# Kernel tuning notes

Hardware: AMD Instinct MI355X
Metric: run time of the kernel (lower is better)

## Reference

```python
import jax, jax.numpy as jnp
import numpy as np

B, D, H, K = 32768, 256, 8192, 32  # tokens, d_in, hidden latents, topk
EPS = float(np.finfo(np.float32).eps)


def setup_inputs() -> dict:
    key = jax.random.key(0)
    k0, k1, k2 = jax.random.split(key, 3)
    x = jax.random.normal(k0, (B, D), jnp.float32)
    W_enc = jax.random.normal(k1, (H, D), jnp.float32) * 0.02
    b_enc = jnp.zeros((H,), jnp.float32)
    # decoder initialized as encoder clone with unit-norm rows (set_decoder_norm_to_unit_norm)
    W_dec0 = jax.random.normal(k2, (H, D), jnp.float32) * 0.02
    W_dec = W_dec0 / (jnp.linalg.norm(W_dec0, axis=1, keepdims=True) + EPS)
    b_dec = jnp.zeros((D,), jnp.float32)
    return {"x": x, "W_enc": W_enc, "b_enc": b_enc, "W_dec": W_dec, "b_dec": b_dec}


def reference(x, W_enc, b_enc, W_dec, b_dec):
    # sae_in = x - b_dec; pre_acts = relu(encoder(sae_in))
    sae_in = x - b_dec
    pre_acts = jax.nn.relu(sae_in @ W_enc.T + b_enc)  # [B, H]
    # topk_activation: keep top-K values per row, zeros elsewhere; then z @ W_dec.
    # Equivalent (same math, no dense scatter): gather the K active decoder rows
    # and take the weighted sum.
    vals, idx = jax.lax.top_k(pre_acts, K)              # [B, K]
    x_reconstructed = jnp.einsum('bk,bkd->bd', vals, W_dec[idx]) + b_dec  # [B, D]
    return x_reconstructed
```

## Files before the change

### kernel.cpp

```cpp
#include <hip/hip_runtime.h>

#define B_TOK 32768
#define D_IN  256
#define H_LAT 8192
#define TOPK  32
#define MT    64
#define NT    128
#define NCH   (H_LAT / NT)
#define CAP   144
#define DELTA 0.016f

typedef __attribute__((ext_vector_type(4))) float f32x4;
typedef __attribute__((ext_vector_type(8))) short bf16x8;

__device__ __forceinline__ unsigned short f2bf(float f) {
    unsigned u = __float_as_uint(f);
    return (unsigned short)((u + 0x7fffu + ((u >> 16) & 1u)) >> 16);
}
__device__ __forceinline__ float bf2f(unsigned short u) {
    return __uint_as_float((unsigned)u << 16);
}

__global__ __launch_bounds__(256)
void conv_kernel(const float* __restrict__ W, unsigned short* __restrict__ Wbf,
                 float* __restrict__ s2w, const float* __restrict__ Wd,
                 unsigned short* __restrict__ Wdbf) {
    const int tid  = threadIdx.x;
    const int wave = tid >> 6, lane = tid & 63;
    const int l15 = lane & 15, quad = lane >> 4;
    const int ct16 = blockIdx.x * 4 + wave;

    float acc = 0.0f;
    {
        const float* src = W + (size_t)(ct16 * 16 + l15) * D_IN + quad * 8;
        unsigned short* dst = Wbf + ((size_t)ct16 * 8) * 512 + lane * 8;
#pragma unroll
        for (int c8 = 0; c8 < 8; ++c8) {
            const float4 v0 = *(const float4*)(src + c8 * 32);
            const float4 v1 = *(const float4*)(src + c8 * 32 + 4);
            acc += v0.x * v0.x + v0.y * v0.y + v0.z * v0.z + v0.w * v0.w +
                   v1.x * v1.x + v1.y * v1.y + v1.z * v1.z + v1.w * v1.w;
            ushort4 p0, p1;
            p0.x = f2bf(v0.x); p0.y = f2bf(v0.y); p0.z = f2bf(v0.z); p0.w = f2bf(v0.w);
            p1.x = f2bf(v1.x); p1.y = f2bf(v1.y); p1.z = f2bf(v1.z); p1.w = f2bf(v1.w);
            *(ushort4*)(dst + c8 * 512)     = p0;
            *(ushort4*)(dst + c8 * 512 + 4) = p1;
        }
    }
    {
        const int total4 = (H_LAT * D_IN) / 4;
        for (int i = blockIdx.x * blockDim.x + tid; i < total4; i += 128 * 256) {
            const float4 d = ((const float4*)Wd)[i];
            ushort4 od;
            od.x = f2bf(d.x); od.y = f2bf(d.y); od.z = f2bf(d.z); od.w = f2bf(d.w);
            ((ushort4*)Wdbf)[i] = od;
        }
    }
#pragma unroll
    for (int off = 32; off > 0; off >>= 1) acc += __shfl_down(acc, off, 64);
    if (lane == 0) atomicAdd(s2w, acc);
}

__global__ __launch_bounds__(512, 4)
void sae_main(const float* __restrict__ x, const float* __restrict__ W_enc,
              const float* __restrict__ b_enc, const float* __restrict__ b_dec,
              float* __restrict__ out,
              const unsigned short* __restrict__ Wbf, const float* __restrict__ s2w,
              const unsigned short* __restrict__ Wdbf) {
    __shared__ __align__(16) char smem[32768 + MT * CAP * 4];
    __shared__ int   cnt[MT];
    __shared__ float thr[MT];

    unsigned short* A = (unsigned short*)smem;
    auto pool = reinterpret_cast<unsigned (*)[CAP]>(smem + 32768);
    unsigned short* ext_i = (unsigned short*)smem;
    float*          ext_v = (float*)(smem + 1024);

    const int tid  = threadIdx.x;
    const int row0 = blockIdx.x * MT;
    const int wave = tid >> 6, lane = tid & 63;
    const int l15 = lane & 15, quad = lane >> 4;

    if (tid < MT) { cnt[tid] = 0; thr[tid] = 0.0f; }
    __syncthreads();

    {
        const int r = tid >> 3, q = tid & 7;
        const float* xr = x + (size_t)(row0 + r) * D_IN + q * 32;
        const float* bd = b_dec + q * 32;
        unsigned short* dst = A + ((r >> 4) * 8 + q) * 512 + (r & 15) * 8;
        float s2 = 0.0f;
#pragma unroll
        for (int j = 0; j < 4; ++j) {
            const float4 a = ((const float4*)xr)[2 * j];
            const float4 b = ((const float4*)xr)[2 * j + 1];
            const float4 da = ((const float4*)bd)[2 * j];
            const float4 db = ((const float4*)bd)[2 * j + 1];
            float v[8] = {a.x - da.x, a.y - da.y, a.z - da.z, a.w - da.w,
                          b.x - db.x, b.y - db.y, b.z - db.z, b.w - db.w};
            ushort4 p0, p1;
            p0.x = f2bf(v[0]); p0.y = f2bf(v[1]); p0.z = f2bf(v[2]); p0.w = f2bf(v[3]);
            p1.x = f2bf(v[4]); p1.y = f2bf(v[5]); p1.z = f2bf(v[6]); p1.w = f2bf(v[7]);
#pragma unroll
            for (int e = 0; e < 8; ++e) s2 += v[e] * v[e];
            *(ushort4*)(dst + j * 128)     = p0;
            *(ushort4*)(dst + j * 128 + 4) = p1;
        }
        atomicAdd(&thr[r], s2);
    }
    __syncthreads();
    if (tid < MT) {
        const float s2wm = s2w[0] * (1.0f / ((float)H_LAT * (float)D_IN));
        thr[tid] = 2.3f * sqrtf(s2wm * thr[tid]);
    }
    __syncthreads();

    float thrv[4][4];
#pragma unroll
    for (int mt = 0; mt < 4; ++mt)
#pragma unroll
        for (int qi = 0; qi < 4; ++qi) thrv[mt][qi] = thr[mt * 16 + quad * 4 + qi];

    const unsigned short* bp = Wbf + (size_t)(wave * 8) * 512 + lane * 8;
    const unsigned short* ap = A + lane * 8;
    const float* bep = b_enc + wave * 16 + l15;
    int col0 = wave * 16 + l15;

    int pos[4][4];
    auto collect = [&](const f32x4 (&ac)[4], int cbase) {
        const unsigned colk = (unsigned)(8191 - cbase);
#pragma unroll
        for (int mt = 0; mt < 4; ++mt)
#pragma unroll
            for (int qi = 0; qi < 4; ++qi) {
                pos[mt][qi] = -1;
                if (ac[mt][qi] > thrv[mt][qi])
                    pos[mt][qi] = atomicAdd(&cnt[mt * 16 + quad * 4 + qi], 1);
            }
#pragma unroll
        for (int mt = 0; mt < 4; ++mt)
#pragma unroll
            for (int qi = 0; qi < 4; ++qi) {
                if ((unsigned)pos[mt][qi] < CAP)
                    pool[mt * 16 + quad * 4 + qi][pos[mt][qi]] =
                        ((unsigned)f2bf(ac[mt][qi]) << 13) | colk;
            }
    };

    for (int g = 0; g < NCH; g += 4) {
        const float bv0 = bep[0],      bv1 = bep[NT];
        const float bv2 = bep[2 * NT], bv3 = bep[3 * NT];

        f32x4 acc0[4], acc1[4], acc2[4], acc3[4];
#pragma unroll
        for (int mt = 0; mt < 4; ++mt) {
            acc0[mt] = {bv0, bv0, bv0, bv0};
            acc1[mt] = {bv1, bv1, bv1, bv1};
            acc2[mt] = {bv2, bv2, bv2, bv2};
            acc3[mt] = {bv3, bv3, bv3, bv3};
        }

#pragma unroll
        for (int c8 = 0; c8 < 8; ++c8) {
            const bf16x8 a0 = *(const bf16x8*)(ap + (0 * 8 + c8) * 512);
            const bf16x8 a1 = *(const bf16x8*)(ap + (1 * 8 + c8) * 512);
            const bf16x8 a2 = *(const bf16x8*)(ap + (2 * 8 + c8) * 512);
            const bf16x8 a3 = *(const bf16x8*)(ap + (3 * 8 + c8) * 512);
            const bf16x8 w0 = *(const bf16x8*)(bp + c8 * 512);
            const bf16x8 w1 = *(const bf16x8*)(bp + 32768 + c8 * 512);
            const bf16x8 w2 = *(const bf16x8*)(bp + 65536 + c8 * 512);
            const bf16x8 w3 = *(const bf16x8*)(bp + 98304 + c8 * 512);
            acc0[0] = __builtin_amdgcn_mfma_f32_16x16x32_bf16(a0, w0, acc0[0], 0, 0, 0);
            acc0[1] = __builtin_amdgcn_mfma_f32_16x16x32_bf16(a1, w0, acc0[1], 0, 0, 0);
            acc0[2] = __builtin_amdgcn_mfma_f32_16x16x32_bf16(a2, w0, acc0[2], 0, 0, 0);
            acc0[3] = __builtin_amdgcn_mfma_f32_16x16x32_bf16(a3, w0, acc0[3], 0, 0, 0);
            acc1[0] = __builtin_amdgcn_mfma_f32_16x16x32_bf16(a0, w1, acc1[0], 0, 0, 0);
            acc1[1] = __builtin_amdgcn_mfma_f32_16x16x32_bf16(a1, w1, acc1[1], 0, 0, 0);
            acc1[2] = __builtin_amdgcn_mfma_f32_16x16x32_bf16(a2, w1, acc1[2], 0, 0, 0);
            acc1[3] = __builtin_amdgcn_mfma_f32_16x16x32_bf16(a3, w1, acc1[3], 0, 0, 0);
            acc2[0] = __builtin_amdgcn_mfma_f32_16x16x32_bf16(a0, w2, acc2[0], 0, 0, 0);
            acc2[1] = __builtin_amdgcn_mfma_f32_16x16x32_bf16(a1, w2, acc2[1], 0, 0, 0);
            acc2[2] = __builtin_amdgcn_mfma_f32_16x16x32_bf16(a2, w2, acc2[2], 0, 0, 0);
            acc2[3] = __builtin_amdgcn_mfma_f32_16x16x32_bf16(a3, w2, acc2[3], 0, 0, 0);
            acc3[0] = __builtin_amdgcn_mfma_f32_16x16x32_bf16(a0, w3, acc3[0], 0, 0, 0);
            acc3[1] = __builtin_amdgcn_mfma_f32_16x16x32_bf16(a1, w3, acc3[1], 0, 0, 0);
            acc3[2] = __builtin_amdgcn_mfma_f32_16x16x32_bf16(a2, w3, acc3[2], 0, 0, 0);
            acc3[3] = __builtin_amdgcn_mfma_f32_16x16x32_bf16(a3, w3, acc3[3], 0, 0, 0);
        }

        collect(acc0, col0);
        collect(acc1, col0 + NT);
        collect(acc2, col0 + 2 * NT);
        collect(acc3, col0 + 3 * NT);

        bp  += 4 * 32768;
        bep += 4 * NT;
        col0 += 4 * NT;
    }
    __syncthreads();

    unsigned short* ei = ext_i + wave * 64;
    float*          ev = ext_v + wave * 64;

    for (int rr = 0; rr < 8; ++rr) {
        const int r = wave * 8 + rr;
        const int n = min(cnt[r], CAP);

        unsigned p[3]; int rk[3];
        const int S = (n <= 128) ? 2 : 3;
#pragma unroll
        for (int e = 0; e < 3; ++e) {
            const int c = e * 64 + lane;
            p[e] = (c < n) ? pool[r][c] : (unsigned)(c + 1);
            rk[e] = 0;
        }
        if (S == 2) {
            for (int s = 0; s < 64; ++s) {
                const int src = (lane + s) & 63;
                const unsigned q0 = (unsigned)__shfl((int)p[0], src, 64);
                const unsigned q1 = (unsigned)__shfl((int)p[1], src, 64);
                rk[0] += (q0 > p[0]) + (q1 > p[0]);
                rk[1] += (q0 > p[1]) + (q1 > p[1]);
            }
        } else {
            for (int s = 0; s < 64; ++s) {
                const int src = (lane + s) & 63;
#pragma unroll
                for (int e = 0; e < 3; ++e) {
                    const unsigned q = (unsigned)__shfl((int)p[e], src, 64);
#pragma unroll
                    for (int a = 0; a < 3; ++a) rk[a] += (q > p[a]);
                }
            }
        }
#pragma unroll
        for (int e = 0; e < 3; ++e) {
            if (e < S && rk[e] < 64) {
                if (p[e] >= 8192u) {
                    ei[rk[e]] = (unsigned short)(8191 - (p[e] & 0x1fffu));
                    ev[rk[e]] = __uint_as_float((p[e] >> 13) << 16);
                } else {
                    ei[rk[e]] = (unsigned short)(0x2000 + rk[e]);
                    ev[rk[e]] = 0.0f;
                }
            }
        }

        const float v32 = ev[TOPK - 1];
        const float va  = ev[lane];
        const int   h   = ei[lane];
        float v = va;
        if (h < H_LAT && fabsf(va - v32) <= DELTA) {
            const float* xr  = x + (size_t)(row0 + r) * D_IN;
            const float* wr_ = W_enc + (size_t)h * D_IN;
            float s = 0.0f;
            for (int kk = 0; kk < D_IN / 4; ++kk) {
                const float4 xv = ((const float4*)xr)[kk];
                const float4 dv = ((const float4*)b_dec)[kk];
                const float4 wv = ((const float4*)wr_)[kk];
                s = fmaf(xv.x - dv.x, wv.x, s);
                s = fmaf(xv.y - dv.y, wv.y, s);
                s = fmaf(xv.z - dv.z, wv.z, s);
                s = fmaf(xv.w - dv.w, wv.w, s);
            }
            v = fmaxf(s + b_enc[h], 0.0f);
        }

        int rank = 0;
        for (int s = 0; s < 64; ++s) {
            const int src = (lane + s) & 63;
            const float wv = __shfl(v, src, 64);
            const int   wh = __shfl(h, src, 64);
            rank += (wv > v) || (wv == v && wh < h);
        }
        if (rank < TOPK) { ev[rank] = v; ei[rank] = (unsigned short)h; }

        const float4 bd4 = *(const float4*)&b_dec[lane * 4];
        float4 o = bd4;
#pragma unroll 8
        for (int k = 0; k < TOPK; ++k) {
            const float vv = ev[k];
            const int   hh = ei[k];
            if (hh < H_LAT) {
                const ushort4 w = *(const ushort4*)&Wdbf[(size_t)hh * D_IN + lane * 4];
                o.x = fmaf(vv, bf2f(w.x), o.x); o.y = fmaf(vv, bf2f(w.y), o.y);
                o.z = fmaf(vv, bf2f(w.z), o.z); o.w = fmaf(vv, bf2f(w.w), o.w);
            }
        }
        *(float4*)&out[(size_t)(row0 + r) * D_IN + lane * 4] = o;
    }
}

extern "C" void kernel_launch(void* const* d_in, const int* in_sizes, int n_in,
                              void* d_out, int out_size, void* d_ws, size_t ws_size,
                              hipStream_t stream) {
    const float* x     = (const float*)d_in[0];
    const float* W_enc = (const float*)d_in[1];
    const float* b_enc = (const float*)d_in[2];
    const float* W_dec = (const float*)d_in[3];
    const float* b_dec = (const float*)d_in[4];
    float* out = (float*)d_out;

    const size_t wel = (size_t)H_LAT * D_IN;
    float* s2w = (float*)d_ws;
    unsigned short* Wbf  = (unsigned short*)((char*)d_ws + 256);
    unsigned short* Wdbf = Wbf + wel;

    hipMemsetAsync(d_ws, 0, 256, stream);
    conv_kernel<<<dim3(128), dim3(256), 0, stream>>>(W_enc, Wbf, s2w, W_dec, Wdbf);
    sae_main<<<dim3(B_TOK / MT), dim3(512), 0, stream>>>(x, W_enc, b_enc, b_dec,
                                                         out, Wbf, s2w, Wdbf);
}
```

Baseline: 546.9 us.

## Software-pipeline encoder weight loads and widen conversion kernel grid

The main loop now handles two 128-column chunks per iteration instead of four. The weight fragments for the next k-step are prefetched into double-buffered registers while the current MFMAs run, which hides global load latency and lowers accumulator register pressure. The conversion kernel is relaunched with 512 blocks, each block splitting one 16-row tile across its waves, so the weight casts have more parallelism. The exact-refinement dot product loop is also unrolled. The risks are a different register allocation and more collect calls per chunk of work.

```diff
diff --git a/kernel.cpp b/kernel.cpp
--- a/kernel.cpp
+++ b/kernel.cpp
@@ -28,14 +28,15 @@
     const int tid  = threadIdx.x;
     const int wave = tid >> 6, lane = tid & 63;
     const int l15 = lane & 15, quad = lane >> 4;
-    const int ct16 = blockIdx.x * 4 + wave;
+    const int ct16 = blockIdx.x;
 
     float acc = 0.0f;
     {
         const float* src = W + (size_t)(ct16 * 16 + l15) * D_IN + quad * 8;
-        unsigned short* dst = Wbf + ((size_t)ct16 * 8) * 512 + lane * 8;
-#pragma unroll
-        for (int c8 = 0; c8 < 8; ++c8) {
+        unsigned short* dst = Wbf + (size_t)ct16 * 4096 + lane * 8;
+#pragma unroll
+        for (int cc = 0; cc < 2; ++cc) {
+            const int c8 = wave * 2 + cc;
             const float4 v0 = *(const float4*)(src + c8 * 32);
             const float4 v1 = *(const float4*)(src + c8 * 32 + 4);
             acc += v0.x * v0.x + v0.y * v0.y + v0.z * v0.z + v0.w * v0.w +
@@ -49,7 +50,7 @@
     }
     {
         const int total4 = (H_LAT * D_IN) / 4;
-        for (int i = blockIdx.x * blockDim.x + tid; i < total4; i += 128 * 256) {
+        for (int i = blockIdx.x * 256 + tid; i < total4; i += 512 * 256) {
             const float4 d = ((const float4*)Wd)[i];
             ushort4 od;
             od.x = f2bf(d.x); od.y = f2bf(d.y); od.z = f2bf(d.z); od.w = f2bf(d.w);
@@ -60,6 +61,24 @@
     for (int off = 32; off > 0; off >>= 1) acc += __shfl_down(acc, off, 64);
     if (lane == 0) atomicAdd(s2w, acc);
 }
+
+#define GSTEP(CW0, CW1, NW0, NW1, C8, NBASE, NC8)                              \
+    {                                                                          \
+        NW0 = *(const bf16x8*)((NBASE) + (NC8) * 512);                         \
+        NW1 = *(const bf16x8*)((NBASE) + 32768 + (NC8) * 512);                 \
+        const bf16x8 a0 = *(const bf16x8*)(ap + (0 * 8 + (C8)) * 512);         \
+        const bf16x8 a1 = *(const bf16x8*)(ap + (1 * 8 + (C8)) * 512);         \
+        const bf16x8 a2 = *(const bf16x8*)(ap + (2 * 8 + (C8)) * 512);         \
+        const bf16x8 a3 = *(const bf16x8*)(ap + (3 * 8 + (C8)) * 512);         \
+        acc0[0] = __builtin_amdgcn_mfma_f32_16x16x32_bf16(a0, CW0, acc0[0], 0, 0, 0); \
+        acc0[1] = __builtin_amdgcn_mfma_f32_16x16x32_bf16(a1, CW0, acc0[1], 0, 0, 0); \
+        acc0[2] = __builtin_amdgcn_mfma_f32_16x16x32_bf16(a2, CW0, acc0[2], 0, 0, 0); \
+        acc0[3] = __builtin_amdgcn_mfma_f32_16x16x32_bf16(a3, CW0, acc0[3], 0, 0, 0); \
+        acc1[0] = __builtin_amdgcn_mfma_f32_16x16x32_bf16(a0, CW1, acc1[0], 0, 0, 0); \
+        acc1[1] = __builtin_amdgcn_mfma_f32_16x16x32_bf16(a1, CW1, acc1[1], 0, 0, 0); \
+        acc1[2] = __builtin_amdgcn_mfma_f32_16x16x32_bf16(a2, CW1, acc1[2], 0, 0, 0); \
+        acc1[3] = __builtin_amdgcn_mfma_f32_16x16x32_bf16(a3, CW1, acc1[3], 0, 0, 0); \
+    }
 
 __global__ __launch_bounds__(512, 4)
 void sae_main(const float* __restrict__ x, const float* __restrict__ W_enc,
@@ -147,55 +166,35 @@
             }
     };
 
-    for (int g = 0; g < NCH; g += 4) {
-        const float bv0 = bep[0],      bv1 = bep[NT];
-        const float bv2 = bep[2 * NT], bv3 = bep[3 * NT];
-
-        f32x4 acc0[4], acc1[4], acc2[4], acc3[4];
+    bf16x8 wa0, wa1, wb0, wb1;
+    wa0 = *(const bf16x8*)(bp);
+    wa1 = *(const bf16x8*)(bp + 32768);
+
+    for (int g = 0; g < NCH; g += 2) {
+        const float bv0 = bep[0], bv1 = bep[NT];
+
+        f32x4 acc0[4], acc1[4];
 #pragma unroll
         for (int mt = 0; mt < 4; ++mt) {
             acc0[mt] = {bv0, bv0, bv0, bv0};
             acc1[mt] = {bv1, bv1, bv1, bv1};
-            acc2[mt] = {bv2, bv2, bv2, bv2};
-            acc3[mt] = {bv3, bv3, bv3, bv3};
-        }
-
-#pragma unroll
-        for (int c8 = 0; c8 < 8; ++c8) {
-            const bf16x8 a0 = *(const bf16x8*)(ap + (0 * 8 + c8) * 512);
-            const bf16x8 a1 = *(const bf16x8*)(ap + (1 * 8 + c8) * 512);
-            const bf16x8 a2 = *(const bf16x8*)(ap + (2 * 8 + c8) * 512);
-            const bf16x8 a3 = *(const bf16x8*)(ap + (3 * 8 + c8) * 512);
-            const bf16x8 w0 = *(const bf16x8*)(bp + c8 * 512);
-            const bf16x8 w1 = *(const bf16x8*)(bp + 32768 + c8 * 512);
-            const bf16x8 w2 = *(const bf16x8*)(bp + 65536 + c8 * 512);
-            const bf16x8 w3 = *(const bf16x8*)(bp + 98304 + c8 * 512);
-            acc0[0] = __builtin_amdgcn_mfma_f32_16x16x32_bf16(a0, w0, acc0[0], 0, 0, 0);
-            acc0[1] = __builtin_amdgcn_mfma_f32_16x16x32_bf16(a1, w0, acc0[1], 0, 0, 0);
-            acc0[2] = __builtin_amdgcn_mfma_f32_16x16x32_bf16(a2, w0, acc0[2], 0, 0, 0);
-            acc0[3] = __builtin_amdgcn_mfma_f32_16x16x32_bf16(a3, w0, acc0[3], 0, 0, 0);
-            acc1[0] = __builtin_amdgcn_mfma_f32_16x16x32_bf16(a0, w1, acc1[0], 0, 0, 0);
-            acc1[1] = __builtin_amdgcn_mfma_f32_16x16x32_bf16(a1, w1, acc1[1], 0, 0, 0);
-            acc1[2] = __builtin_amdgcn_mfma_f32_16x16x32_bf16(a2, w1, acc1[2], 0, 0, 0);
-            acc1[3] = __builtin_amdgcn_mfma_f32_16x16x32_bf16(a3, w1, acc1[3], 0, 0, 0);
-            acc2[0] = __builtin_amdgcn_mfma_f32_16x16x32_bf16(a0, w2, acc2[0], 0, 0, 0);
-            acc2[1] = __builtin_amdgcn_mfma_f32_16x16x32_bf16(a1, w2, acc2[1], 0, 0, 0);
-            acc2[2] = __builtin_amdgcn_mfma_f32_16x16x32_bf16(a2, w2, acc2[2], 0, 0, 0);
-            acc2[3] = __builtin_amdgcn_mfma_f32_16x16x32_bf16(a3, w2, acc2[3], 0, 0, 0);
-            acc3[0] = __builtin_amdgcn_mfma_f32_16x16x32_bf16(a0, w3, acc3[0], 0, 0, 0);
-            acc3[1] = __builtin_amdgcn_mfma_f32_16x16x32_bf16(a1, w3, acc3[1], 0, 0, 0);
-            acc3[2] = __builtin_amdgcn_mfma_f32_16x16x32_bf16(a2, w3, acc3[2], 0, 0, 0);
-            acc3[3] = __builtin_amdgcn_mfma_f32_16x16x32_bf16(a3, w3, acc3[3], 0, 0, 0);
-        }
+        }
+
+        GSTEP(wa0, wa1, wb0, wb1, 0, bp, 1);
+        GSTEP(wb0, wb1, wa0, wa1, 1, bp, 2);
+        GSTEP(wa0, wa1, wb0, wb1, 2, bp, 3);
+        GSTEP(wb0, wb1, wa0, wa1, 3, bp, 4);
+        GSTEP(wa0, wa1, wb0, wb1, 4, bp, 5);
+        GSTEP(wb0, wb1, wa0, wa1, 5, bp, 6);
+        GSTEP(wa0, wa1, wb0, wb1, 6, bp, 7);
+        GSTEP(wb0, wb1, wa0, wa1, 7, bp + 65536, 0);
 
         collect(acc0, col0);
         collect(acc1, col0 + NT);
-        collect(acc2, col0 + 2 * NT);
-        collect(acc3, col0 + 3 * NT);
-
-        bp  += 4 * 32768;
-        bep += 4 * NT;
-        col0 += 4 * NT;
+
+        bp  += 65536;
+        bep += 2 * NT;
+        col0 += 2 * NT;
     }
     __syncthreads();
 
@@ -254,6 +253,7 @@
             const float* xr  = x + (size_t)(row0 + r) * D_IN;
             const float* wr_ = W_enc + (size_t)h * D_IN;
             float s = 0.0f;
+#pragma unroll 16
             for (int kk = 0; kk < D_IN / 4; ++kk) {
                 const float4 xv = ((const float4*)xr)[kk];
                 const float4 dv = ((const float4*)b_dec)[kk];
@@ -307,7 +307,7 @@
     unsigned short* Wdbf = Wbf + wel;
 
     hipMemsetAsync(d_ws, 0, 256, stream);
-    conv_kernel<<<dim3(128), dim3(256), 0, stream>>>(W_enc, Wbf, s2w, W_dec, Wdbf);
+    conv_kernel<<<dim3(512), dim3(256), 0, stream>>>(W_enc, Wbf, s2w, W_dec, Wdbf);
     sae_main<<<dim3(B_TOK / MT), dim3(512), 0, stream>>>(x, W_enc, b_enc, b_dec,
                                                          out, Wbf, s2w, Wdbf);
 }
```

Measured after the change: 517.0 us. -5.5%, faster.
